# Optimization experiments

Hardware: AMD Instinct MI355X
Metric: run time of the kernel (lower is better)

The kernel has to match this reference:

```python
import jax, jax.numpy as jnp
import numpy as np

EPS = 1e-6
TAU = 0.07


def setup_inputs() -> dict:
    key = jax.random.key(0)
    kx, ky = jax.random.split(key)
    B, D = 4096, 1024
    x = jax.random.normal(kx, (B, D), dtype=jnp.float32)
    y = jax.random.normal(ky, (B, D), dtype=jnp.float32)
    return {"x": x, "y": y}


def reference(x, y):
    B = x.shape[0]
    # torch CosineSimilarity: dot / (max(||x||, eps) * max(||y||, eps))
    xn = x / jnp.maximum(jnp.linalg.norm(x, axis=-1, keepdims=True), EPS)
    yn = y / jnp.maximum(jnp.linalg.norm(y, axis=-1, keepdims=True), EPS)
    S = jnp.einsum('id,jd->ij', xn, yn)          # [B, B] cosine sims, S[i,j]=cos(x_i,y_j)
    E = jnp.exp(S / TAU)                          # bounded: |S|<=1 so exp <= e^{1/0.07}
    diag = jnp.diagonal(E)
    # original: sum_j (exp + eps) + eps  ->  sum_j exp + B*eps + eps
    extra = B * EPS + EPS
    row_denom = jnp.sum(E, axis=1) + extra        # x->y direction (loop 1)
    col_denom = jnp.sum(E, axis=0) + extra        # y->x direction (loop 2)
    coef = -1.0 / (2.0 * B)
    loss = coef * (jnp.sum(jnp.log(diag / row_denom)) + jnp.sum(jnp.log(diag / col_denom)))
    return loss
```

## Files before the change

kernel.cpp:

```cpp
#include <hip/hip_runtime.h>
#include <hip/hip_bf16.h>

#define NB 4096
#define DK 1024
#define EPSF 1e-6f
#define QSCALE 16.0f

typedef __attribute__((ext_vector_type(8))) int   i32x8_t;
typedef __attribute__((ext_vector_type(4))) int   i32x4_t;
typedef __attribute__((ext_vector_type(4))) float f32x4_t;

__device__ __forceinline__ void async16(const void* g, void* lds) {
    __builtin_amdgcn_global_load_lds(
        (const __attribute__((address_space(1))) void*)g,
        (__attribute__((address_space(3))) void*)lds, 16, 0, 0);
}

__global__ __launch_bounds__(256) void normalize_rows(
    const float* __restrict__ x, const float* __restrict__ y,
    unsigned* __restrict__ xq, unsigned* __restrict__ yq,
    float* __restrict__ sdiag, float* __restrict__ zerobuf)
{
    const int t = threadIdx.x;
    const int gid = blockIdx.x * 256 + t;
    if (gid < 2 * NB) zerobuf[gid] = 0.f;

    const int wave = t >> 6;
    const int lane = t & 63;
    const int row  = blockIdx.x * 4 + wave;

    const float4* xr = reinterpret_cast<const float4*>(x + (size_t)row * DK);
    const float4* yr = reinterpret_cast<const float4*>(y + (size_t)row * DK);

    float4 xv[4], yv[4];
    float ssx = 0.f, ssy = 0.f, sxy = 0.f;
    #pragma unroll
    for (int j = 0; j < 4; ++j) {
        xv[j] = xr[j * 64 + lane];
        yv[j] = yr[j * 64 + lane];
        ssx += xv[j].x*xv[j].x + xv[j].y*xv[j].y + xv[j].z*xv[j].z + xv[j].w*xv[j].w;
        ssy += yv[j].x*yv[j].x + yv[j].y*yv[j].y + yv[j].z*yv[j].z + yv[j].w*yv[j].w;
        sxy += xv[j].x*yv[j].x + xv[j].y*yv[j].y + xv[j].z*yv[j].z + xv[j].w*yv[j].w;
    }
    #pragma unroll
    for (int off = 1; off < 64; off <<= 1) {
        ssx += __shfl_xor(ssx, off, 64);
        ssy += __shfl_xor(ssy, off, 64);
        sxy += __shfl_xor(sxy, off, 64);
    }
    const float invx = 1.0f / fmaxf(sqrtf(ssx), EPSF);
    const float invy = 1.0f / fmaxf(sqrtf(ssy), EPSF);
    const float sx = invx * QSCALE;
    const float sy = invy * QSCALE;

    unsigned* xw = xq + (size_t)row * 256;
    unsigned* yw = yq + (size_t)row * 256;
    #pragma unroll
    for (int j = 0; j < 4; ++j) {
        int px = __builtin_amdgcn_cvt_pk_fp8_f32(xv[j].x * sx, xv[j].y * sx, 0, false);
        px     = __builtin_amdgcn_cvt_pk_fp8_f32(xv[j].z * sx, xv[j].w * sx, px, true);
        int py = __builtin_amdgcn_cvt_pk_fp8_f32(yv[j].x * sy, yv[j].y * sy, 0, false);
        py     = __builtin_amdgcn_cvt_pk_fp8_f32(yv[j].z * sy, yv[j].w * sy, py, true);
        xw[j * 64 + lane] = (unsigned)px;
        yw[j * 64 + lane] = (unsigned)py;
    }
    if (lane == 0) sdiag[row] = sxy * invx * invy;
}

__global__ __launch_bounds__(256) void gemm_exp_sums(
    const unsigned char* __restrict__ xq, const unsigned char* __restrict__ yq,
    float* __restrict__ rowsum, float* __restrict__ colsum)
{
    __shared__ __align__(16) unsigned char At[128 * 128];
    __shared__ __align__(16) unsigned char Bt[128 * 128];

    const int t    = threadIdx.x;
    const int lane = t & 63;
    const int wave = t >> 6;
    const int q    = lane >> 4;
    const int l15  = lane & 15;
    const int h    = l15 & 7;

    const int R0 = blockIdx.y * 128;
    const int C0 = blockIdx.x * 128;
    const int wRow = (wave >> 1) * 64;
    const int wCol = (wave & 1) * 64;

    f32x4_t acc[4][4];
    #pragma unroll
    for (int i = 0; i < 4; i++)
        #pragma unroll
        for (int j = 0; j < 4; j++)
            acc[i][j] = (f32x4_t){0.f, 0.f, 0.f, 0.f};

    const int r8  = lane >> 3;
    const int gsw = (lane & 7) ^ r8;
    const unsigned char* pA = xq + (size_t)(R0 + wave * 32 + r8) * DK + gsw * 16;
    const unsigned char* pB = yq + (size_t)(C0 + wave * 32 + r8) * DK + gsw * 16;

    const unsigned char* baseALo = &At[(wRow + l15) * 128 + (((2*q)    ) ^ h) * 16];
    const unsigned char* baseAHi = &At[(wRow + l15) * 128 + (((2*q) + 1) ^ h) * 16];
    const unsigned char* baseBLo = &Bt[(wCol + l15) * 128 + (((2*q)    ) ^ h) * 16];
    const unsigned char* baseBHi = &Bt[(wCol + l15) * 128 + (((2*q) + 1) ^ h) * 16];

    #pragma unroll 1
    for (int kb = 0; kb < DK; kb += 128) {
        __syncthreads();
        #pragma unroll
        for (int c = 0; c < 4; ++c) {
            async16(pA + c * 8192, &At[(wave * 32 + c * 8) * 128]);
            async16(pB + c * 8192, &Bt[(wave * 32 + c * 8) * 128]);
        }
        pA += 128;
        pB += 128;
        __syncthreads();

        i32x8_t bfr[4];
        #pragma unroll
        for (int nt = 0; nt < 4; ++nt) {
            const i32x4_t lo = *reinterpret_cast<const i32x4_t*>(baseBLo + nt * 2048);
            const i32x4_t hi = *reinterpret_cast<const i32x4_t*>(baseBHi + nt * 2048);
            bfr[nt][0] = lo[0]; bfr[nt][1] = lo[1]; bfr[nt][2] = lo[2]; bfr[nt][3] = lo[3];
            bfr[nt][4] = hi[0]; bfr[nt][5] = hi[1]; bfr[nt][6] = hi[2]; bfr[nt][7] = hi[3];
        }
        #pragma unroll
        for (int mt = 0; mt < 4; ++mt) {
            const i32x4_t lo = *reinterpret_cast<const i32x4_t*>(baseALo + mt * 2048);
            const i32x4_t hi = *reinterpret_cast<const i32x4_t*>(baseAHi + mt * 2048);
            i32x8_t af;
            af[0] = lo[0]; af[1] = lo[1]; af[2] = lo[2]; af[3] = lo[3];
            af[4] = hi[0]; af[5] = hi[1]; af[6] = hi[2]; af[7] = hi[3];
            #pragma unroll
            for (int nt = 0; nt < 4; ++nt)
                acc[mt][nt] = __builtin_amdgcn_mfma_scale_f32_16x16x128_f8f6f4(
                    af, bfr[nt], acc[mt][nt],
                    0, 0,
                    0, 0x7F7F7F7F,
                    0, 0x7F7F7F7F);
        }
    }

    const float kScale = (float)(1.0 / (256.0 * 0.07 * 0.6931471805599453));
    float csum[4] = {0.f, 0.f, 0.f, 0.f};
    #pragma unroll
    for (int mt = 0; mt < 4; ++mt) {
        float rsum[4] = {0.f, 0.f, 0.f, 0.f};
        #pragma unroll
        for (int nt = 0; nt < 4; ++nt) {
            #pragma unroll
            for (int r = 0; r < 4; ++r) {
                const float e = exp2f(acc[mt][nt][r] * kScale);
                rsum[r]  += e;
                csum[nt] += e;
            }
        }
        #pragma unroll
        for (int r = 0; r < 4; ++r) {
            float v = rsum[r];
            v += __shfl_xor(v, 1, 64);
            v += __shfl_xor(v, 2, 64);
            v += __shfl_xor(v, 4, 64);
            v += __shfl_xor(v, 8, 64);
            if (l15 == 0)
                atomicAdd(&rowsum[R0 + wRow + mt * 16 + q * 4 + r], v);
        }
    }
    #pragma unroll
    for (int nt = 0; nt < 4; ++nt) {
        float v = csum[nt];
        v += __shfl_xor(v, 16, 64);
        v += __shfl_xor(v, 32, 64);
        if (lane < 16)
            atomicAdd(&colsum[C0 + wCol + nt * 16 + l15], v);
    }
}

__global__ __launch_bounds__(1024) void finalize(
    const float* __restrict__ rowsum, const float* __restrict__ colsum,
    const float* __restrict__ sdiag, float* __restrict__ out)
{
    const float extra = (float)(NB * 1e-6 + 1e-6);
    double local = 0.0;
    for (int i = threadIdx.x; i < NB; i += 1024) {
        local += (double)sdiag[i] * (2.0 / 0.07)
               - (double)logf(rowsum[i] + extra)
               - (double)logf(colsum[i] + extra);
    }
    #pragma unroll
    for (int off = 1; off < 64; off <<= 1)
        local += __shfl_xor(local, off, 64);
    __shared__ double dred[16];
    const int wave = threadIdx.x >> 6;
    if ((threadIdx.x & 63) == 0) dred[wave] = local;
    __syncthreads();
    if (threadIdx.x == 0) {
        double tot = 0.0;
        #pragma unroll
        for (int w = 0; w < 16; ++w) tot += dred[w];
        out[0] = (float)(tot * (-1.0 / (2.0 * NB)));
    }
}

extern "C" void kernel_launch(void* const* d_in, const int* in_sizes, int n_in,
                              void* d_out, int out_size, void* d_ws, size_t ws_size,
                              hipStream_t stream)
{
    const float* x = (const float*)d_in[0];
    const float* y = (const float*)d_in[1];
    float* out = (float*)d_out;

    char* ws = (char*)d_ws;
    unsigned char* xq = (unsigned char*)ws;
    unsigned char* yq = (unsigned char*)(ws + (size_t)4 * 1024 * 1024);
    float* rowsum = (float*)(ws + (size_t)8 * 1024 * 1024);
    float* colsum = rowsum + NB;
    float* sdiag  = colsum + NB;

    normalize_rows<<<NB / 4, 256, 0, stream>>>(x, y, (unsigned*)xq, (unsigned*)yq,
                                               sdiag, rowsum);

    dim3 grid(NB / 128, NB / 128);
    gemm_exp_sums<<<grid, 256, 0, stream>>>(xq, yq, rowsum, colsum);

    finalize<<<1, 1024, 0, stream>>>(rowsum, colsum, sdiag, out);
}
```

Baseline: 113.0 us.

## Pre-tile FP8 operands in MFMA fragment order and load directly from global

The normalize kernel now writes the quantized FP8 rows in a tiled layout that matches the MFMA 16x16x128 fragment order, so each lane's 32 bytes sit contiguously. The GEMM kernel drops its LDS staging and both per-iteration barriers and reads fragments straight from global memory. This removes the sync and LDS traffic but gives up LDS reuse between waves, so operand reuse now depends on L1/L2 hits, and there is no software prefetch across k iterations.

```diff
diff --git a/kernel.cpp b/kernel.cpp
--- a/kernel.cpp
+++ b/kernel.cpp
@@ -10,11 +10,6 @@
 typedef __attribute__((ext_vector_type(4))) int   i32x4_t;
 typedef __attribute__((ext_vector_type(4))) float f32x4_t;
 
-__device__ __forceinline__ void async16(const void* g, void* lds) {
-    __builtin_amdgcn_global_load_lds(
-        (const __attribute__((address_space(1))) void*)g,
-        (__attribute__((address_space(3))) void*)lds, 16, 0, 0);
-}
 
 __global__ __launch_bounds__(256) void normalize_rows(
     const float* __restrict__ x, const float* __restrict__ y,
@@ -53,16 +48,19 @@
     const float sx = invx * QSCALE;
     const float sy = invy * QSCALE;
 
-    unsigned* xw = xq + (size_t)row * 256;
-    unsigned* yw = yq + (size_t)row * 256;
+    const int p = row >> 4, r = row & 15;
+    const int qs = (lane >> 3) & 3;
+    const int bs = (lane & 7) * 4;
     #pragma unroll
     for (int j = 0; j < 4; ++j) {
+        const int kb = j * 2 + (lane >> 5);
+        const unsigned off = ((unsigned)(p * 32 + kb * 4 + qs) * 512 + r * 32 + bs) >> 2;
         int px = __builtin_amdgcn_cvt_pk_fp8_f32(xv[j].x * sx, xv[j].y * sx, 0, false);
         px     = __builtin_amdgcn_cvt_pk_fp8_f32(xv[j].z * sx, xv[j].w * sx, px, true);
         int py = __builtin_amdgcn_cvt_pk_fp8_f32(yv[j].x * sy, yv[j].y * sy, 0, false);
         py     = __builtin_amdgcn_cvt_pk_fp8_f32(yv[j].z * sy, yv[j].w * sy, py, true);
-        xw[j * 64 + lane] = (unsigned)px;
-        yw[j * 64 + lane] = (unsigned)py;
+        xq[off] = (unsigned)px;
+        yq[off] = (unsigned)py;
     }
     if (lane == 0) sdiag[row] = sxy * invx * invy;
 }
@@ -71,15 +69,11 @@
     const unsigned char* __restrict__ xq, const unsigned char* __restrict__ yq,
     float* __restrict__ rowsum, float* __restrict__ colsum)
 {
-    __shared__ __align__(16) unsigned char At[128 * 128];
-    __shared__ __align__(16) unsigned char Bt[128 * 128];
-
     const int t    = threadIdx.x;
     const int lane = t & 63;
     const int wave = t >> 6;
     const int q    = lane >> 4;
     const int l15  = lane & 15;
-    const int h    = l15 & 7;
 
     const int R0 = blockIdx.y * 128;
     const int C0 = blockIdx.x * 128;
@@ -93,40 +87,28 @@
         for (int j = 0; j < 4; j++)
             acc[i][j] = (f32x4_t){0.f, 0.f, 0.f, 0.f};
 
-    const int r8  = lane >> 3;
-    const int gsw = (lane & 7) ^ r8;
-    const unsigned char* pA = xq + (size_t)(R0 + wave * 32 + r8) * DK + gsw * 16;
-    const unsigned char* pB = yq + (size_t)(C0 + wave * 32 + r8) * DK + gsw * 16;
-
-    const unsigned char* baseALo = &At[(wRow + l15) * 128 + (((2*q)    ) ^ h) * 16];
-    const unsigned char* baseAHi = &At[(wRow + l15) * 128 + (((2*q) + 1) ^ h) * 16];
-    const unsigned char* baseBLo = &Bt[(wCol + l15) * 128 + (((2*q)    ) ^ h) * 16];
-    const unsigned char* baseBHi = &Bt[(wCol + l15) * 128 + (((2*q) + 1) ^ h) * 16];
+    const unsigned char* Abase =
+        xq + (size_t)(((R0 + wRow) >> 4) * 32 + q) * 512 + l15 * 32;
+    const unsigned char* Bbase =
+        yq + (size_t)(((C0 + wCol) >> 4) * 32 + q) * 512 + l15 * 32;
 
     #pragma unroll 1
-    for (int kb = 0; kb < DK; kb += 128) {
-        __syncthreads();
-        #pragma unroll
-        for (int c = 0; c < 4; ++c) {
-            async16(pA + c * 8192, &At[(wave * 32 + c * 8) * 128]);
-            async16(pB + c * 8192, &Bt[(wave * 32 + c * 8) * 128]);
-        }
-        pA += 128;
-        pB += 128;
-        __syncthreads();
+    for (int kb = 0; kb < 8; ++kb) {
+        const unsigned char* Ak = Abase + kb * 2048;
+        const unsigned char* Bk = Bbase + kb * 2048;
 
         i32x8_t bfr[4];
         #pragma unroll
         for (int nt = 0; nt < 4; ++nt) {
-            const i32x4_t lo = *reinterpret_cast<const i32x4_t*>(baseBLo + nt * 2048);
-            const i32x4_t hi = *reinterpret_cast<const i32x4_t*>(baseBHi + nt * 2048);
+            const i32x4_t lo = *reinterpret_cast<const i32x4_t*>(Bk + nt * 16384);
+            const i32x4_t hi = *reinterpret_cast<const i32x4_t*>(Bk + nt * 16384 + 16);
             bfr[nt][0] = lo[0]; bfr[nt][1] = lo[1]; bfr[nt][2] = lo[2]; bfr[nt][3] = lo[3];
             bfr[nt][4] = hi[0]; bfr[nt][5] = hi[1]; bfr[nt][6] = hi[2]; bfr[nt][7] = hi[3];
         }
         #pragma unroll
         for (int mt = 0; mt < 4; ++mt) {
-            const i32x4_t lo = *reinterpret_cast<const i32x4_t*>(baseALo + mt * 2048);
-            const i32x4_t hi = *reinterpret_cast<const i32x4_t*>(baseAHi + mt * 2048);
+            const i32x4_t lo = *reinterpret_cast<const i32x4_t*>(Ak + mt * 16384);
+            const i32x4_t hi = *reinterpret_cast<const i32x4_t*>(Ak + mt * 16384 + 16);
             i32x8_t af;
             af[0] = lo[0]; af[1] = lo[1]; af[2] = lo[2]; af[3] = lo[3];
             af[4] = hi[0]; af[5] = hi[1]; af[6] = hi[2]; af[7] = hi[3];
```

After: 112.1 us. Within noise of the previous version (-0.8%).
